# Kernel tuning notes

Hardware: AMD Instinct MI355X
Metric: run time of the kernel (lower is better)

The kernel has to match this reference:

```python
import jax, jax.numpy as jnp
import numpy as np

GROUPS = 32
EPS = 1e-5


def setup_inputs() -> dict:
    key = jax.random.key(0)
    ks = jax.random.split(key, 11)
    B, C, H, W = 64, 256, 32, 32
    s = 1.0 / np.sqrt(C)  # conv1d k=1 init scale
    inp = {
        'x': jax.random.normal(ks[0], (B, C, H, W), jnp.float32),
        'gn_weight': jnp.ones((C,), jnp.float32),
        'gn_bias': jnp.zeros((C,), jnp.float32),
        'wq': jax.random.uniform(ks[1], (C, C), jnp.float32, -s, s),
        'bq': jax.random.uniform(ks[2], (C,), jnp.float32, -s, s),
        'wk': jax.random.uniform(ks[3], (C, C), jnp.float32, -s, s),
        'bk': jax.random.uniform(ks[4], (C,), jnp.float32, -s, s),
        'wv': jax.random.uniform(ks[5], (C, C), jnp.float32, -s, s),
        'bv': jax.random.uniform(ks[6], (C,), jnp.float32, -s, s),
        'wo': jax.random.uniform(ks[7], (C, C), jnp.float32, -s, s),
        'bo': jax.random.uniform(ks[8], (C,), jnp.float32, -s, s),
    }
    return inp


def _group_norm(x, weight, bias):
    # x: (B, C, H, W); normalize per (group-channels, H, W)
    B, C, H, W = x.shape
    xg = x.reshape(B, GROUPS, C // GROUPS, H, W)
    mean = xg.mean(axis=(2, 3, 4), keepdims=True)
    var = xg.var(axis=(2, 3, 4), keepdims=True)
    xg = (xg - mean) * jax.lax.rsqrt(var + EPS)
    xn = xg.reshape(B, C, H, W)
    return xn * weight[None, :, None, None] + bias[None, :, None, None]


def reference(x, gn_weight, gn_bias, wq, bq, wk, bk, wv, bv, wo, bo):
    B, C, H, W = x.shape
    h = _group_norm(x, gn_weight, gn_bias).reshape(B, C, H * W)  # (B,C,N)
    # 1x1 conv1d == per-position linear over channels
    q = jnp.einsum('oc,bcn->bon', wq, h) + bq[None, :, None]
    k = jnp.einsum('oc,bcn->bon', wk, h) + bk[None, :, None]
    v = jnp.einsum('oc,bcn->bon', wv, h) + bv[None, :, None]
    scores = jnp.einsum('bcn,bcm->bnm', q, k) * (C ** -0.5)  # (B,N,N)
    weights = jax.nn.softmax(scores, axis=-1)
    attn = jnp.einsum('bnm,bcm->bcn', weights, v)  # (B,C,N)
    out = jnp.einsum('oc,bcn->bon', wo, attn) + bo[None, :, None]
    return x + out.reshape(B, C, H, W)
```

## Files before the change

kernel.cpp:

```cpp
#include <hip/hip_runtime.h>


#define BB 64
#define CC 256
#define NN 1024

typedef float  floatx4  __attribute__((ext_vector_type(4)));
typedef short  shortx8  __attribute__((ext_vector_type(8)));
typedef unsigned short ushortx4 __attribute__((ext_vector_type(4)));
typedef unsigned short ushortx8 __attribute__((ext_vector_type(8)));

__device__ __forceinline__ unsigned short f2bf(float f) {
  union { float f; unsigned int u; } cv; cv.f = f;
  unsigned int u = cv.u;
  u += 0x7fffu + ((u >> 16) & 1u);
  return (unsigned short)(u >> 16);
}

__device__ __forceinline__ floatx4 mfma16(shortx8 a, shortx8 b, floatx4 c) {
  return __builtin_amdgcn_mfma_f32_16x16x32_bf16(a, b, c, 0, 0, 0);
}

__device__ __forceinline__ void gload16(const unsigned short* g, unsigned short* s) {
  __builtin_amdgcn_global_load_lds(
      reinterpret_cast<const __attribute__((address_space(1))) void*>(
          (unsigned long long)g),
      reinterpret_cast<__attribute__((address_space(3))) void*>(
          (unsigned int)(unsigned long long)s),
      16, 0, 0);
}

__device__ __forceinline__ void barrier_raw() {
  asm volatile("" ::: "memory");
  __builtin_amdgcn_s_barrier();
  asm volatile("" ::: "memory");
}

__device__ __forceinline__ void bar_lds() {
  asm volatile("s_waitcnt lgkmcnt(0)" ::: "memory");
  __builtin_amdgcn_sched_barrier(0);
  barrier_raw();
}

__device__ __forceinline__ int sigma32(int r) {
  return (((r >> 2) & 3) << 3) + (((r >> 4) & 1) << 2) + (r & 3);
}

__global__ __launch_bounds__(256) void gn_kernel(const float* __restrict__ x,
                                                 const float* __restrict__ gw,
                                                 const float* __restrict__ gb,
                                                 unsigned short* __restrict__ h_t,
                                                 const float* __restrict__ wq, const float* __restrict__ bq,
                                                 const float* __restrict__ wk, const float* __restrict__ bk,
                                                 const float* __restrict__ wv, const float* __restrict__ bv,
                                                 const float* __restrict__ wo,
                                                 unsigned short* __restrict__ wqkv,
                                                 unsigned short* __restrict__ wo_bf,
                                                 float* __restrict__ bqkv) {
  if (blockIdx.x >= 32) {
    int cid = (blockIdx.x - 32) * 64 + blockIdx.y;
    int i = cid * 256 + threadIdx.x;
    if (i < 196608) {
      int o = i >> 8, c = i & 255;
      float val;
      if (o < 256)      val = wq[o * 256 + c] * 0.0625f;
      else if (o < 512) val = wk[(o - 256) * 256 + c];
      else              val = wv[(o - 512) * 256 + c];
      wqkv[i] = f2bf(val);
    } else if (i < 262144) {
      int j = i - 196608;
      wo_bf[j] = f2bf(wo[j]);
    } else if (i < 262912) {
      int o = i - 262144;
      float val;
      if (o < 256)      val = bq[o] * 0.0625f;
      else if (o < 512) val = bk[o - 256];
      else              val = bv[o - 512];
      bqkv[o] = val;
    }
    return;
  }
  int g = blockIdx.x, b = blockIdx.y;
  int t = threadIdx.x;
  const float* xb = x + ((size_t)b * CC + g * 8) * NN;

  float vals[8][4];
  float s = 0.f, sq = 0.f;
#pragma unroll
  for (int cc = 0; cc < 8; cc++) {
    floatx4 v4 = *(const floatx4*)(xb + cc * NN + t * 4);
#pragma unroll
    for (int j = 0; j < 4; j++) {
      vals[cc][j] = v4[j];
      s += v4[j];
      sq += v4[j] * v4[j];
    }
  }
#pragma unroll
  for (int d = 1; d < 64; d <<= 1) {
    s  += __shfl_xor(s, d);
    sq += __shfl_xor(sq, d);
  }
  __shared__ float ssum[4], ssq[4];
  int w = t >> 6;
  if ((t & 63) == 0) { ssum[w] = s; ssq[w] = sq; }
  __syncthreads();
  s  = ssum[0] + ssum[1] + ssum[2] + ssum[3];
  sq = ssq[0] + ssq[1] + ssq[2] + ssq[3];
  float mean = s * (1.f / 8192.f);
  float var  = sq * (1.f / 8192.f) - mean * mean;
  float rstd = rsqrtf(var + 1e-5f);

  float gam[8], bet[8];
#pragma unroll
  for (int cc = 0; cc < 8; cc++) {
    float gm = gw[g * 8 + cc] * rstd;
    gam[cc] = gm;
    bet[cc] = gb[g * 8 + cc] - mean * gm;
  }
  unsigned short* hb = h_t + (size_t)b * NN * CC + g * 8;
#pragma unroll
  for (int j = 0; j < 4; j++) {
    ushortx8 pk;
#pragma unroll
    for (int cc = 0; cc < 8; cc++) pk[cc] = f2bf(vals[cc][j] * gam[cc] + bet[cc]);
    *(ushortx8*)(hb + (size_t)(t * 4 + j) * CC) = pk;
  }
}

__global__ __launch_bounds__(512, 4) void qkv_gemm(const unsigned short* __restrict__ h_t,
                                                   const unsigned short* __restrict__ wqkv,
                                                   const float* __restrict__ bqkv,
                                                   unsigned short* __restrict__ q_t,
                                                   unsigned short* __restrict__ k_t,
                                                   unsigned short* __restrict__ v) {
  __shared__ __align__(16) unsigned short sM[32768];
  __shared__ __align__(16) unsigned short sRep[32 * 136];
  int rb = blockIdx.x, b = blockIdx.y;
  int t = threadIdx.x, w = t >> 6, l = t & 63, lo = l & 15, h = l >> 4;
  int rowg = w >> 1, colg = w & 1;
  const unsigned short* A = h_t + ((size_t)b * NN + rb * 128) * CC;

  int srow_w = w * 2 + (l >> 5);
  int schunk = l & 31;

#pragma unroll
  for (int i = 0; i < 8; i++) {
    int row = i * 16 + srow_w;
    gload16(A + (size_t)row * CC + ((schunk ^ (row & 7)) << 3),
            &sM[(i * 16 + w * 2) << 8]);
  }
  asm volatile("s_waitcnt vmcnt(0)" ::: "memory");
  barrier_raw();

  shortx8 a[2][8];
#pragma unroll
  for (int i = 0; i < 2; i++) {
    int row = rowg * 32 + i * 16 + lo;
#pragma unroll
    for (int ch = 0; ch < 8; ch++)
      a[i][ch] = *(const shortx8*)(&sM[(row << 8) + (((ch * 4 + h) ^ (row & 7)) << 3)]);
  }
  bar_lds();

#pragma unroll
  for (int i = 0; i < 4; i++) {
    int row = i * 16 + srow_w;
    gload16(wqkv + (size_t)row * CC + ((schunk ^ (row & 7)) << 3),
            &sM[(i * 16 + w * 2) << 8]);
  }

  floatx4 zero4 = {0.f, 0.f, 0.f, 0.f};
  for (int c = 0; c < 12; c++) {
    int cb = (c & 1) << 14;
    if (c < 11) {
      int nb = ((c + 1) & 1) << 14;
#pragma unroll
      for (int i = 0; i < 4; i++) {
        int row = i * 16 + srow_w;
        gload16(wqkv + (size_t)((c + 1) * 64 + row) * CC + ((schunk ^ (row & 7)) << 3),
                &sM[nb + ((i * 16 + w * 2) << 8)]);
      }
      asm volatile("s_waitcnt vmcnt(4)" ::: "memory");
    } else {
      asm volatile("s_waitcnt vmcnt(0)" ::: "memory");
    }
    barrier_raw();

    floatx4 acc[2][2];
    acc[0][0] = zero4; acc[0][1] = zero4; acc[1][0] = zero4; acc[1][1] = zero4;
    int r0 = colg * 32 + lo, r1 = colg * 32 + 16 + lo;
    __builtin_amdgcn_s_setprio(1);
#pragma unroll
    for (int ch = 0; ch < 8; ch++) {
      shortx8 b0 = *(const shortx8*)(&sM[cb + (r0 << 8) + (((ch * 4 + h) ^ (r0 & 7)) << 3)]);
      shortx8 b1 = *(const shortx8*)(&sM[cb + (r1 << 8) + (((ch * 4 + h) ^ (r1 & 7)) << 3)]);
      acc[0][0] = mfma16(a[0][ch], b0, acc[0][0]);
      acc[0][1] = mfma16(a[0][ch], b1, acc[0][1]);
      acc[1][0] = mfma16(a[1][ch], b0, acc[1][0]);
      acc[1][1] = mfma16(a[1][ch], b1, acc[1][1]);
    }
    __builtin_amdgcn_s_setprio(0);

    if (c < 8) {
      unsigned short* dst = (c < 4) ? q_t : k_t;
      bar_lds();
      unsigned short* sQK = &sM[cb];
#pragma unroll
      for (int i = 0; i < 2; i++) {
#pragma unroll
        for (int j = 0; j < 2; j++) {
          float bias = bqkv[(c << 6) + colg * 32 + j * 16 + lo];
          int o_l = colg * 32 + j * 16 + lo;
#pragma unroll
          for (int r = 0; r < 4; r++) {
            int n_l = rowg * 32 + i * 16 + h * 4 + r;
            sQK[n_l * 72 + o_l] = f2bf(acc[i][j][r] + bias);
          }
        }
      }
      bar_lds();
#pragma unroll
      for (int p = 0; p < 2; p++) {
        int slot = p * 512 + t;
        int n_l = slot >> 3, sg = (slot & 7) << 3;
        ushortx8 vv = *(const ushortx8*)(&sQK[n_l * 72 + sg]);
        *(ushortx8*)(dst + ((size_t)b * NN + rb * 128 + n_l) * CC + ((c & 3) << 6) + sg) = vv;
      }
      bar_lds();
    } else {
      int vch0 = (c - 8) << 6;
#pragma unroll
      for (int half = 0; half < 2; half++) {
        if (colg == half) {
#pragma unroll
          for (int i = 0; i < 2; i++) {
#pragma unroll
            for (int j = 0; j < 2; j++) {
              float bias = bqkv[512 + vch0 + half * 32 + j * 16 + lo];
              ushortx4 pk;
#pragma unroll
              for (int r = 0; r < 4; r++) pk[r] = f2bf(acc[i][j][r] + bias);
              *(ushortx4*)(&sRep[(j * 16 + lo) * 136 + rowg * 32 + i * 16 + h * 4]) = pk;
            }
          }
        }
        bar_lds();
        int o_l = t >> 4, nseg = (t & 15) << 3;
        ushortx8 vv = *(const ushortx8*)(&sRep[o_l * 136 + nseg]);
        *(ushortx8*)(v + ((size_t)b * CC + vch0 + half * 32 + o_l) * NN + rb * 128 + nseg) = vv;
        bar_lds();
      }
    }
  }
}

__global__ __launch_bounds__(512, 2) void flash_kernel(const unsigned short* __restrict__ q_t,
                                                       const unsigned short* __restrict__ k_t,
                                                       const unsigned short* __restrict__ v,
                                                       unsigned short* __restrict__ attn_t) {
  __shared__ __align__(16) unsigned short sMem[32768];
  int bid = blockIdx.x;
  int wgid = ((bid & 7) << 5) + (bid >> 3);
  int b = wgid >> 2, qblk = wgid & 3;
  int t = threadIdx.x, w = t >> 6, l = t & 63, lo = l & 15, h = l >> 4;
  const unsigned short* qtb = q_t + (size_t)b * NN * CC;
  const unsigned short* ktb = k_t + (size_t)b * NN * CC;
  const unsigned short* vb  = v   + (size_t)b * CC * NN;
  int qbase = qblk * 256 + w * 32;

  shortx8 qfA[8], qfB[8];
#pragma unroll
  for (int ch = 0; ch < 8; ch++) {
    qfA[ch] = *(const shortx8*)(qtb + (size_t)(qbase + lo) * CC + ch * 32 + h * 8);
    qfB[ch] = *(const shortx8*)(qtb + (size_t)(qbase + 16 + lo) * CC + ch * 32 + h * 8);
  }

  floatx4 zero4 = {0.f, 0.f, 0.f, 0.f};
  floatx4 oA[16], oB[16];
#pragma unroll
  for (int i = 0; i < 16; i++) { oA[i] = zero4; oB[i] = zero4; }
  float mA = -1e30f, lsA = 0.f, mB = -1e30f, lsB = 0.f;

  int krow_l = (w << 2) + (l >> 5);
  int kchunk = l & 31;
  int vrow_l = (w << 5) + (l >> 2);
  int vchunk = l & 3;

#pragma unroll
  for (int i = 0; i < 2; i++) {
    int row = krow_l + i * 2;
    gload16(ktb + (size_t)sigma32(row) * CC + ((kchunk ^ (row & 7)) << 3),
            &sMem[((w << 2) + i * 2) << 8]);
  }
#pragma unroll
  for (int i = 0; i < 2; i++) {
    int row = vrow_l + i * 16;
    gload16(vb + (size_t)row * NN + ((vchunk ^ ((row >> 1) & 3)) << 3),
            &sMem[16384 + (((w << 5) + i * 16) << 5)]);
  }

  for (int kb = 0; kb < 32; kb++) {
    int cur = kb & 1;
    int kB = cur << 13;
    int vB = 16384 + (cur << 13);
    if (kb < 31) {
      int nxt = cur ^ 1, k0n = (kb + 1) << 5;
#pragma unroll
      for (int i = 0; i < 2; i++) {
        int row = krow_l + i * 2;
        gload16(ktb + (size_t)(k0n + sigma32(row)) * CC + ((kchunk ^ (row & 7)) << 3),
                &sMem[(nxt << 13) + (((w << 2) + i * 2) << 8)]);
      }
#pragma unroll
      for (int i = 0; i < 2; i++) {
        int row = vrow_l + i * 16;
        gload16(vb + (size_t)row * NN + k0n + ((vchunk ^ ((row >> 1) & 3)) << 3),
                &sMem[16384 + (nxt << 13) + (((w << 5) + i * 16) << 5)]);
      }
      asm volatile("s_waitcnt vmcnt(4)" ::: "memory");
    } else {
      asm volatile("s_waitcnt vmcnt(0)" ::: "memory");
    }
    barrier_raw();

    floatx4 sA[2], sB[2];
#pragma unroll
    for (int i = 0; i < 2; i++) { sA[i] = zero4; sB[i] = zero4; }
    __builtin_amdgcn_s_setprio(1);
#pragma unroll
    for (int kt = 0; kt < 2; kt++) {
      const unsigned short* kp = &sMem[kB + ((kt * 16 + lo) << 8)];
#pragma unroll
      for (int ch = 0; ch < 8; ch++) {
        shortx8 kf = *(const shortx8*)(kp + (((ch * 4 + h) ^ (lo & 7)) << 3));
        sA[kt] = mfma16(kf, qfA[ch], sA[kt]);
        sB[kt] = mfma16(kf, qfB[ch], sB[kt]);
      }
    }
    __builtin_amdgcn_s_setprio(0);

    unsigned int pkA[2][2], pkB[2][2];
    {
      float pmax = fmaxf(fmaxf(fmaxf(sA[0][0], sA[0][1]), fmaxf(sA[0][2], sA[0][3])),
                         fmaxf(fmaxf(sA[1][0], sA[1][1]), fmaxf(sA[1][2], sA[1][3])));
      if (!__all(pmax - mA <= 8.f)) {
        pmax = fmaxf(pmax, __shfl_xor(pmax, 16));
        pmax = fmaxf(pmax, __shfl_xor(pmax, 32));
        float mn = fmaxf(mA, pmax);
        float alpha = __expf(mA - mn);
        mA = mn;
        lsA *= alpha;
#pragma unroll
        for (int r = 0; r < 4; r++) {
          float ar = __shfl(alpha, (h << 4) + (h << 2) + r);
#pragma unroll
          for (int cbi = 0; cbi < 16; cbi++) oA[cbi][r] *= ar;
        }
      }
      float rs = 0.f;
#pragma unroll
      for (int kt = 0; kt < 2; kt++) {
        float p0 = __expf(sA[kt][0] - mA);
        float p1 = __expf(sA[kt][1] - mA);
        float p2 = __expf(sA[kt][2] - mA);
        float p3 = __expf(sA[kt][3] - mA);
        rs += (p0 + p1) + (p2 + p3);
        pkA[kt][0] = (unsigned)f2bf(p0) | ((unsigned)f2bf(p1) << 16);
        pkA[kt][1] = (unsigned)f2bf(p2) | ((unsigned)f2bf(p3) << 16);
      }
      lsA += rs;
    }
    {
      float pmax = fmaxf(fmaxf(fmaxf(sB[0][0], sB[0][1]), fmaxf(sB[0][2], sB[0][3])),
                         fmaxf(fmaxf(sB[1][0], sB[1][1]), fmaxf(sB[1][2], sB[1][3])));
      if (!__all(pmax - mB <= 8.f)) {
        pmax = fmaxf(pmax, __shfl_xor(pmax, 16));
        pmax = fmaxf(pmax, __shfl_xor(pmax, 32));
        float mn = fmaxf(mB, pmax);
        float alpha = __expf(mB - mn);
        mB = mn;
        lsB *= alpha;
#pragma unroll
        for (int r = 0; r < 4; r++) {
          float ar = __shfl(alpha, (h << 4) + (h << 2) + r);
#pragma unroll
          for (int cbi = 0; cbi < 16; cbi++) oB[cbi][r] *= ar;
        }
      }
      float rs = 0.f;
#pragma unroll
      for (int kt = 0; kt < 2; kt++) {
        float p0 = __expf(sB[kt][0] - mB);
        float p1 = __expf(sB[kt][1] - mB);
        float p2 = __expf(sB[kt][2] - mB);
        float p3 = __expf(sB[kt][3] - mB);
        rs += (p0 + p1) + (p2 + p3);
        pkB[kt][0] = (unsigned)f2bf(p0) | ((unsigned)f2bf(p1) << 16);
        pkB[kt][1] = (unsigned)f2bf(p2) | ((unsigned)f2bf(p3) << 16);
      }
      lsB += rs;
    }

    {
      union { unsigned int u[4]; shortx8 v; } paA, paB;
      paA.u[0] = pkA[0][0]; paA.u[1] = pkA[0][1];
      paA.u[2] = pkA[1][0]; paA.u[3] = pkA[1][1];
      paB.u[0] = pkB[0][0]; paB.u[1] = pkB[0][1];
      paB.u[2] = pkB[1][0]; paB.u[3] = pkB[1][1];
      __builtin_amdgcn_s_setprio(1);
#pragma unroll
      for (int cbi = 0; cbi < 16; cbi++) {
        int row = (cbi << 4) + lo;
        shortx8 vf = *(const shortx8*)(&sMem[vB + (row << 5) +
                                             ((h ^ ((row >> 1) & 3)) << 3)]);
        oA[cbi] = mfma16(paA.v, vf, oA[cbi]);
        oB[cbi] = mfma16(paB.v, vf, oB[cbi]);
      }
      __builtin_amdgcn_s_setprio(0);
    }
    barrier_raw();
  }

  lsA += __shfl_xor(lsA, 16);
  lsA += __shfl_xor(lsA, 32);
  lsB += __shfl_xor(lsB, 16);
  lsB += __shfl_xor(lsB, 32);

  float rlA[4], rlB[4];
#pragma unroll
  for (int r = 0; r < 4; r++) {
    rlA[r] = 1.f / __shfl(lsA, (h << 4) + (h << 2) + r);
    rlB[r] = 1.f / __shfl(lsB, (h << 4) + (h << 2) + r);
  }
  unsigned short* ab = attn_t + (size_t)b * NN * CC;
  unsigned short* ow = &sMem[w << 12];

#pragma unroll
  for (int cbi = 0; cbi < 16; cbi++) {
#pragma unroll
    for (int r = 0; r < 4; r++) {
      int q = (h << 2) + r;
      int c = (cbi << 4) + lo;
      int sw = (q ^ (q >> 3)) & 7;
      ow[(q << 8) + (((c >> 3) ^ sw) << 3) + (lo & 7)] = f2bf(oA[cbi][r] * rlA[r]);
    }
  }
  bar_lds();
#pragma unroll
  for (int it = 0; it < 8; it++) {
    int q = (it << 1) + (l >> 5);
    int gc = l & 31;
    int sw = (q ^ (q >> 3)) & 7;
    ushortx8 vv = *(const ushortx8*)(&ow[(q << 8) + ((gc ^ sw) << 3)]);
    *(ushortx8*)(ab + (size_t)(qbase + q) * CC + (gc << 3)) = vv;
  }
  bar_lds();
#pragma unroll
  for (int cbi = 0; cbi < 16; cbi++) {
#pragma unroll
    for (int r = 0; r < 4; r++) {
      int q = (h << 2) + r;
      int c = (cbi << 4) + lo;
      int sw = (q ^ (q >> 3)) & 7;
      ow[(q << 8) + (((c >> 3) ^ sw) << 3) + (lo & 7)] = f2bf(oB[cbi][r] * rlB[r]);
    }
  }
  bar_lds();
#pragma unroll
  for (int it = 0; it < 8; it++) {
    int q = (it << 1) + (l >> 5);
    int gc = l & 31;
    int sw = (q ^ (q >> 3)) & 7;
    ushortx8 vv = *(const ushortx8*)(&ow[(q << 8) + ((gc ^ sw) << 3)]);
    *(ushortx8*)(ab + (size_t)(qbase + 16 + q) * CC + (gc << 3)) = vv;
  }
}

__global__ __launch_bounds__(512, 4) void outproj_gemm(const unsigned short* __restrict__ attn_t,
                                                       const unsigned short* __restrict__ wo_bf,
                                                       const float* __restrict__ bo,
                                                       const float* __restrict__ x,
                                                       float* __restrict__ out) {
  __shared__ __align__(16) unsigned short sM[32768];
  __shared__ __align__(16) float sRepF[16 * 132];
  int rb = blockIdx.x, b = blockIdx.y;
  int t = threadIdx.x, w = t >> 6, l = t & 63, lo = l & 15, h = l >> 4;
  int rowg = w >> 1, colg = w & 1;
  const unsigned short* A = attn_t + ((size_t)b * NN + rb * 128) * CC;

  int srow_w = w * 2 + (l >> 5);
  int schunk = l & 31;

#pragma unroll
  for (int i = 0; i < 8; i++) {
    int row = i * 16 + srow_w;
    gload16(A + (size_t)row * CC + ((schunk ^ (row & 7)) << 3),
            &sM[(i * 16 + w * 2) << 8]);
  }
  asm volatile("s_waitcnt vmcnt(0)" ::: "memory");
  barrier_raw();

  shortx8 a[2][8];
#pragma unroll
  for (int i = 0; i < 2; i++) {
    int row = rowg * 32 + i * 16 + lo;
#pragma unroll
    for (int ch = 0; ch < 8; ch++)
      a[i][ch] = *(const shortx8*)(&sM[(row << 8) + (((ch * 4 + h) ^ (row & 7)) << 3)]);
  }
  bar_lds();

#pragma unroll
  for (int i = 0; i < 4; i++) {
    int row = i * 16 + srow_w;
    gload16(wo_bf + (size_t)row * CC + ((schunk ^ (row & 7)) << 3),
            &sM[(i * 16 + w * 2) << 8]);
  }

  floatx4 zero4 = {0.f, 0.f, 0.f, 0.f};
  for (int c = 0; c < 4; c++) {
    int cb = (c & 1) << 14;
    if (c < 3) {
      int nb = ((c + 1) & 1) << 14;
#pragma unroll
      for (int i = 0; i < 4; i++) {
        int row = i * 16 + srow_w;
        gload16(wo_bf + (size_t)((c + 1) * 64 + row) * CC + ((schunk ^ (row & 7)) << 3),
                &sM[nb + ((i * 16 + w * 2) << 8)]);
      }
      asm volatile("s_waitcnt vmcnt(4)" ::: "memory");
    } else {
      asm volatile("s_waitcnt vmcnt(0)" ::: "memory");
    }
    barrier_raw();

    floatx4 acc[2][2];
    acc[0][0] = zero4; acc[0][1] = zero4; acc[1][0] = zero4; acc[1][1] = zero4;
    int r0 = colg * 32 + lo, r1 = colg * 32 + 16 + lo;
    __builtin_amdgcn_s_setprio(1);
#pragma unroll
    for (int ch = 0; ch < 8; ch++) {
      shortx8 b0 = *(const shortx8*)(&sM[cb + (r0 << 8) + (((ch * 4 + h) ^ (r0 & 7)) << 3)]);
      shortx8 b1 = *(const shortx8*)(&sM[cb + (r1 << 8) + (((ch * 4 + h) ^ (r1 & 7)) << 3)]);
      acc[0][0] = mfma16(a[0][ch], b0, acc[0][0]);
      acc[0][1] = mfma16(a[0][ch], b1, acc[0][1]);
      acc[1][0] = mfma16(a[1][ch], b0, acc[1][0]);
      acc[1][1] = mfma16(a[1][ch], b1, acc[1][1]);
    }
    __builtin_amdgcn_s_setprio(0);

#pragma unroll
    for (int quarter = 0; quarter < 4; quarter++) {
      int j = quarter & 1;
      if (colg == (quarter >> 1)) {
        float bias = bo[(c << 6) + quarter * 16 + lo];
#pragma unroll
        for (int i = 0; i < 2; i++) {
          floatx4 val;
#pragma unroll
          for (int r = 0; r < 4; r++) val[r] = acc[i][j][r] + bias;
          *(floatx4*)(&sRepF[lo * 132 + rowg * 32 + i * 16 + h * 4]) = val;
        }
      }
      bar_lds();
      int o_l = t >> 5, nq = (t & 31) << 2;
      floatx4 rep = *(const floatx4*)(&sRepF[o_l * 132 + nq]);
      size_t idx = ((size_t)b * CC + (c << 6) + quarter * 16 + o_l) * NN + rb * 128 + nq;
      floatx4 xr = *(const floatx4*)(x + idx);
#pragma unroll
      for (int r = 0; r < 4; r++) rep[r] += xr[r];
      *(floatx4*)(out + idx) = rep;
      bar_lds();
    }
  }
}

extern "C" void kernel_launch(void* const* d_in, const int* in_sizes, int n_in,
                              void* d_out, int out_size, void* d_ws, size_t ws_size,
                              hipStream_t stream) {
  const float* x  = (const float*)d_in[0];
  const float* gw = (const float*)d_in[1];
  const float* gb = (const float*)d_in[2];
  const float* wq = (const float*)d_in[3];
  const float* bq = (const float*)d_in[4];
  const float* wk = (const float*)d_in[5];
  const float* bk = (const float*)d_in[6];
  const float* wv = (const float*)d_in[7];
  const float* bv = (const float*)d_in[8];
  const float* wo = (const float*)d_in[9];
  const float* bo = (const float*)d_in[10];
  float* out = (float*)d_out;

  char* ws = (char*)d_ws;
  unsigned short* q_t   = (unsigned short*)(ws);
  unsigned short* k_t   = (unsigned short*)(ws + 33554432);
  unsigned short* v     = (unsigned short*)(ws + 67108864);
  unsigned short* h_t   = (unsigned short*)(ws + 100663296);
  unsigned short* wqkv  = (unsigned short*)(ws + 134217728);
  unsigned short* wo_bf = (unsigned short*)(ws + 134610944);
  float*          bqkv  = (float*)(ws + 134742016);
  unsigned short* attn_t = h_t;

  gn_kernel<<<dim3(49, 64), dim3(256), 0, stream>>>(x, gw, gb, h_t,
                                                    wq, bq, wk, bk, wv, bv, wo,
                                                    wqkv, wo_bf, bqkv);
  qkv_gemm<<<dim3(8, 64), dim3(512), 0, stream>>>(h_t, wqkv, bqkv, q_t, k_t, v);
  flash_kernel<<<dim3(256), dim3(512), 0, stream>>>(q_t, k_t, v, attn_t);
  outproj_gemm<<<dim3(8, 64), dim3(512), 0, stream>>>(attn_t, wo_bf, bo, x, out);
}
```

Baseline: 189.0 us.

## Quad-buffer K/V tiles and process two key tiles per barrier in flash kernel

The flash attention loop changes from a double-buffered 32-key step to four LDS buffers, handling two 32-key tiles per iteration. This prefetches two tiles ahead and halves the number of barriers and wait points per key sweep. The cost is doubling shared memory to 128 KB per block, which cannot fit two blocks per CU as the launch bounds request, so occupancy likely drops to one block per CU. It also adds register pressure from the extra score accumulators.

```diff
diff --git a/kernel.cpp b/kernel.cpp
--- a/kernel.cpp
+++ b/kernel.cpp
@@ -259,7 +259,7 @@
                                                        const unsigned short* __restrict__ k_t,
                                                        const unsigned short* __restrict__ v,
                                                        unsigned short* __restrict__ attn_t) {
-  __shared__ __align__(16) unsigned short sMem[32768];
+  __shared__ __align__(16) unsigned short sMem[65536];
   int bid = blockIdx.x;
   int wgid = ((bid & 7) << 5) + (bid >> 3);
   int b = wgid >> 2, qblk = wgid & 3;
@@ -288,62 +288,83 @@
   int vchunk = l & 3;
 
 #pragma unroll
-  for (int i = 0; i < 2; i++) {
-    int row = krow_l + i * 2;
-    gload16(ktb + (size_t)sigma32(row) * CC + ((kchunk ^ (row & 7)) << 3),
-            &sMem[((w << 2) + i * 2) << 8]);
-  }
-#pragma unroll
-  for (int i = 0; i < 2; i++) {
-    int row = vrow_l + i * 16;
-    gload16(vb + (size_t)row * NN + ((vchunk ^ ((row >> 1) & 3)) << 3),
-            &sMem[16384 + (((w << 5) + i * 16) << 5)]);
-  }
-
-  for (int kb = 0; kb < 32; kb++) {
-    int cur = kb & 1;
-    int kB = cur << 13;
-    int vB = 16384 + (cur << 13);
-    if (kb < 31) {
-      int nxt = cur ^ 1, k0n = (kb + 1) << 5;
-#pragma unroll
-      for (int i = 0; i < 2; i++) {
-        int row = krow_l + i * 2;
-        gload16(ktb + (size_t)(k0n + sigma32(row)) * CC + ((kchunk ^ (row & 7)) << 3),
-                &sMem[(nxt << 13) + (((w << 2) + i * 2) << 8)]);
-      }
-#pragma unroll
-      for (int i = 0; i < 2; i++) {
-        int row = vrow_l + i * 16;
-        gload16(vb + (size_t)row * NN + k0n + ((vchunk ^ ((row >> 1) & 3)) << 3),
-                &sMem[16384 + (nxt << 13) + (((w << 5) + i * 16) << 5)]);
-      }
-      asm volatile("s_waitcnt vmcnt(4)" ::: "memory");
+  for (int tt = 0; tt < 2; tt++) {
+    int k0 = tt << 5;
+#pragma unroll
+    for (int i = 0; i < 2; i++) {
+      int row = krow_l + i * 2;
+      gload16(ktb + (size_t)(k0 + sigma32(row)) * CC + ((kchunk ^ (row & 7)) << 3),
+              &sMem[(tt << 13) + (((w << 2) + i * 2) << 8)]);
+    }
+#pragma unroll
+    for (int i = 0; i < 2; i++) {
+      int row = vrow_l + i * 16;
+      gload16(vb + (size_t)row * NN + k0 + ((vchunk ^ ((row >> 1) & 3)) << 3),
+              &sMem[32768 + (tt << 13) + (((w << 5) + i * 16) << 5)]);
+    }
+  }
+
+  for (int j = 0; j < 16; j++) {
+    if (j < 15) {
+#pragma unroll
+      for (int tt = 0; tt < 2; tt++) {
+        int kbn = 2 * j + 2 + tt;
+        int k0n = kbn << 5;
+        int bufn = kbn & 3;
+#pragma unroll
+        for (int i = 0; i < 2; i++) {
+          int row = krow_l + i * 2;
+          gload16(ktb + (size_t)(k0n + sigma32(row)) * CC + ((kchunk ^ (row & 7)) << 3),
+                  &sMem[(bufn << 13) + (((w << 2) + i * 2) << 8)]);
+        }
+#pragma unroll
+        for (int i = 0; i < 2; i++) {
+          int row = vrow_l + i * 16;
+          gload16(vb + (size_t)row * NN + k0n + ((vchunk ^ ((row >> 1) & 3)) << 3),
+                  &sMem[32768 + (bufn << 13) + (((w << 5) + i * 16) << 5)]);
+        }
+      }
+      asm volatile("s_waitcnt vmcnt(8)" ::: "memory");
     } else {
       asm volatile("s_waitcnt vmcnt(0)" ::: "memory");
     }
     barrier_raw();
 
-    floatx4 sA[2], sB[2];
-#pragma unroll
-    for (int i = 0; i < 2; i++) { sA[i] = zero4; sB[i] = zero4; }
+    int kBa = ((2 * j) & 3) << 13;
+    int kBb = ((2 * j + 1) & 3) << 13;
+    int vBa = 32768 + (((2 * j) & 3) << 13);
+    int vBb = 32768 + (((2 * j + 1) & 3) << 13);
+
+    floatx4 sAa[2], sBa[2], sAb[2], sBb[2];
+#pragma unroll
+    for (int i = 0; i < 2; i++) { sAa[i] = zero4; sBa[i] = zero4; sAb[i] = zero4; sBb[i] = zero4; }
     __builtin_amdgcn_s_setprio(1);
 #pragma unroll
     for (int kt = 0; kt < 2; kt++) {
-      const unsigned short* kp = &sMem[kB + ((kt * 16 + lo) << 8)];
+      const unsigned short* kp = &sMem[kBa + ((kt * 16 + lo) << 8)];
 #pragma unroll
       for (int ch = 0; ch < 8; ch++) {
         shortx8 kf = *(const shortx8*)(kp + (((ch * 4 + h) ^ (lo & 7)) << 3));
-        sA[kt] = mfma16(kf, qfA[ch], sA[kt]);
-        sB[kt] = mfma16(kf, qfB[ch], sB[kt]);
+        sAa[kt] = mfma16(kf, qfA[ch], sAa[kt]);
+        sBa[kt] = mfma16(kf, qfB[ch], sBa[kt]);
+      }
+    }
+#pragma unroll
+    for (int kt = 0; kt < 2; kt++) {
+      const unsigned short* kp = &sMem[kBb + ((kt * 16 + lo) << 8)];
+#pragma unroll
+      for (int ch = 0; ch < 8; ch++) {
+        shortx8 kf = *(const shortx8*)(kp + (((ch * 4 + h) ^ (lo & 7)) << 3));
+        sAb[kt] = mfma16(kf, qfA[ch], sAb[kt]);
+        sBb[kt] = mfma16(kf, qfB[ch], sBb[kt]);
       }
     }
     __builtin_amdgcn_s_setprio(0);
 
-    unsigned int pkA[2][2], pkB[2][2];
+    unsigned int pkAa[2][2], pkBa[2][2], pkAb[2][2], pkBb[2][2];
     {
-      float pmax = fmaxf(fmaxf(fmaxf(sA[0][0], sA[0][1]), fmaxf(sA[0][2], sA[0][3])),
-                         fmaxf(fmaxf(sA[1][0], sA[1][1]), fmaxf(sA[1][2], sA[1][3])));
+      float pmax = fmaxf(fmaxf(fmaxf(sAa[0][0], sAa[0][1]), fmaxf(sAa[0][2], sAa[0][3])),
+                         fmaxf(fmaxf(sAa[1][0], sAa[1][1]), fmaxf(sAa[1][2], sAa[1][3])));
       if (!__all(pmax - mA <= 8.f)) {
         pmax = fmaxf(pmax, __shfl_xor(pmax, 16));
         pmax = fmaxf(pmax, __shfl_xor(pmax, 32));
@@ -361,19 +382,19 @@
       float rs = 0.f;
 #pragma unroll
       for (int kt = 0; kt < 2; kt++) {
-        float p0 = __expf(sA[kt][0] - mA);
-        float p1 = __expf(sA[kt][1] - mA);
-        float p2 = __expf(sA[kt][2] - mA);
-        float p3 = __expf(sA[kt][3] - mA);
+        float p0 = __expf(sAa[kt][0] - mA);
+        float p1 = __expf(sAa[kt][1] - mA);
+        float p2 = __expf(sAa[kt][2] - mA);
+        float p3 = __expf(sAa[kt][3] - mA);
         rs += (p0 + p1) + (p2 + p3);
-        pkA[kt][0] = (unsigned)f2bf(p0) | ((unsigned)f2bf(p1) << 16);
-        pkA[kt][1] = (unsigned)f2bf(p2) | ((unsigned)f2bf(p3) << 16);
+        pkAa[kt][0] = (unsigned)f2bf(p0) | ((unsigned)f2bf(p1) << 16);
+        pkAa[kt][1] = (unsigned)f2bf(p2) | ((unsigned)f2bf(p3) << 16);
       }
       lsA += rs;
     }
     {
-      float pmax = fmaxf(fmaxf(fmaxf(sB[0][0], sB[0][1]), fmaxf(sB[0][2], sB[0][3])),
-                         fmaxf(fmaxf(sB[1][0], sB[1][1]), fmaxf(sB[1][2], sB[1][3])));
+      float pmax = fmaxf(fmaxf(fmaxf(sBa[0][0], sBa[0][1]), fmaxf(sBa[0][2], sBa[0][3])),
+                         fmaxf(fmaxf(sBa[1][0], sBa[1][1]), fmaxf(sBa[1][2], sBa[1][3])));
       if (!__all(pmax - mB <= 8.f)) {
         pmax = fmaxf(pmax, __shfl_xor(pmax, 16));
         pmax = fmaxf(pmax, __shfl_xor(pmax, 32));
@@ -391,28 +412,104 @@
       float rs = 0.f;
 #pragma unroll
       for (int kt = 0; kt < 2; kt++) {
-        float p0 = __expf(sB[kt][0] - mB);
-        float p1 = __expf(sB[kt][1] - mB);
-        float p2 = __expf(sB[kt][2] - mB);
-        float p3 = __expf(sB[kt][3] - mB);
+        float p0 = __expf(sBa[kt][0] - mB);
+        float p1 = __expf(sBa[kt][1] - mB);
+        float p2 = __expf(sBa[kt][2] - mB);
+        float p3 = __expf(sBa[kt][3] - mB);
         rs += (p0 + p1) + (p2 + p3);
-        pkB[kt][0] = (unsigned)f2bf(p0) | ((unsigned)f2bf(p1) << 16);
-        pkB[kt][1] = (unsigned)f2bf(p2) | ((unsigned)f2bf(p3) << 16);
+        pkBa[kt][0] = (unsigned)f2bf(p0) | ((unsigned)f2bf(p1) << 16);
+        pkBa[kt][1] = (unsigned)f2bf(p2) | ((unsigned)f2bf(p3) << 16);
       }
       lsB += rs;
     }
-
     {
       union { unsigned int u[4]; shortx8 v; } paA, paB;
-      paA.u[0] = pkA[0][0]; paA.u[1] = pkA[0][1];
-      paA.u[2] = pkA[1][0]; paA.u[3] = pkA[1][1];
-      paB.u[0] = pkB[0][0]; paB.u[1] = pkB[0][1];
-      paB.u[2] = pkB[1][0]; paB.u[3] = pkB[1][1];
+      paA.u[0] = pkAa[0][0]; paA.u[1] = pkAa[0][1];
+      paA.u[2] = pkAa[1][0]; paA.u[3] = pkAa[1][1];
+      paB.u[0] = pkBa[0][0]; paB.u[1] = pkBa[0][1];
+      paB.u[2] = pkBa[1][0]; paB.u[3] = pkBa[1][1];
       __builtin_amdgcn_s_setprio(1);
 #pragma unroll
       for (int cbi = 0; cbi < 16; cbi++) {
         int row = (cbi << 4) + lo;
-        shortx8 vf = *(const shortx8*)(&sMem[vB + (row << 5) +
+        shortx8 vf = *(const shortx8*)(&sMem[vBa + (row << 5) +
+                                             ((h ^ ((row >> 1) & 3)) << 3)]);
+        oA[cbi] = mfma16(paA.v, vf, oA[cbi]);
+        oB[cbi] = mfma16(paB.v, vf, oB[cbi]);
+      }
+      __builtin_amdgcn_s_setprio(0);
+    }
+    {
+      float pmax = fmaxf(fmaxf(fmaxf(sAb[0][0], sAb[0][1]), fmaxf(sAb[0][2], sAb[0][3])),
+                         fmaxf(fmaxf(sAb[1][0], sAb[1][1]), fmaxf(sAb[1][2], sAb[1][3])));
+      if (!__all(pmax - mA <= 8.f)) {
+        pmax = fmaxf(pmax, __shfl_xor(pmax, 16));
+        pmax = fmaxf(pmax, __shfl_xor(pmax, 32));
+        float mn = fmaxf(mA, pmax);
+        float alpha = __expf(mA - mn);
+        mA = mn;
+        lsA *= alpha;
+#pragma unroll
+        for (int r = 0; r < 4; r++) {
+          float ar = __shfl(alpha, (h << 4) + (h << 2) + r);
+#pragma unroll
+          for (int cbi = 0; cbi < 16; cbi++) oA[cbi][r] *= ar;
+        }
+      }
+      float rs = 0.f;
+#pragma unroll
+      for (int kt = 0; kt < 2; kt++) {
+        float p0 = __expf(sAb[kt][0] - mA);
+        float p1 = __expf(sAb[kt][1] - mA);
+        float p2 = __expf(sAb[kt][2] - mA);
+        float p3 = __expf(sAb[kt][3] - mA);
+        rs += (p0 + p1) + (p2 + p3);
+        pkAb[kt][0] = (unsigned)f2bf(p0) | ((unsigned)f2bf(p1) << 16);
+        pkAb[kt][1] = (unsigned)f2bf(p2) | ((unsigned)f2bf(p3) << 16);
+      }
+      lsA += rs;
+    }
+    {
+      float pmax = fmaxf(fmaxf(fmaxf(sBb[0][0], sBb[0][1]), fmaxf(sBb[0][2], sBb[0][3])),
+                         fmaxf(fmaxf(sBb[1][0], sBb[1][1]), fmaxf(sBb[1][2], sBb[1][3])));
+      if (!__all(pmax - mB <= 8.f)) {
+        pmax = fmaxf(pmax, __shfl_xor(pmax, 16));
+        pmax = fmaxf(pmax, __shfl_xor(pmax, 32));
+        float mn = fmaxf(mB, pmax);
+        float alpha = __expf(mB - mn);
+        mB = mn;
+        lsB *= alpha;
+#pragma unroll
+        for (int r = 0; r < 4; r++) {
+          float ar = __shfl(alpha, (h << 4) + (h << 2) + r);
+#pragma unroll
+          for (int cbi = 0; cbi < 16; cbi++) oB[cbi][r] *= ar;
+        }
+      }
+      float rs = 0.f;
+#pragma unroll
+      for (int kt = 0; kt < 2; kt++) {
+        float p0 = __expf(sBb[kt][0] - mB);
+        float p1 = __expf(sBb[kt][1] - mB);
+        float p2 = __expf(sBb[kt][2] - mB);
+        float p3 = __expf(sBb[kt][3] - mB);
+        rs += (p0 + p1) + (p2 + p3);
+        pkBb[kt][0] = (unsigned)f2bf(p0) | ((unsigned)f2bf(p1) << 16);
+        pkBb[kt][1] = (unsigned)f2bf(p2) | ((unsigned)f2bf(p3) << 16);
+      }
+      lsB += rs;
+    }
+    {
+      union { unsigned int u[4]; shortx8 v; } paA, paB;
+      paA.u[0] = pkAb[0][0]; paA.u[1] = pkAb[0][1];
+      paA.u[2] = pkAb[1][0]; paA.u[3] = pkAb[1][1];
+      paB.u[0] = pkBb[0][0]; paB.u[1] = pkBb[0][1];
+      paB.u[2] = pkBb[1][0]; paB.u[3] = pkBb[1][1];
+      __builtin_amdgcn_s_setprio(1);
+#pragma unroll
+      for (int cbi = 0; cbi < 16; cbi++) {
+        int row = (cbi << 4) + lo;
+        shortx8 vf = *(const shortx8*)(&sMem[vBb + (row << 5) +
                                              ((h ^ ((row >> 1) & 3)) << 3)]);
         oA[cbi] = mfma16(paA.v, vf, oA[cbi]);
         oB[cbi] = mfma16(paB.v, vf, oB[cbi]);
```

After: 219.5 us. 16.1% more time.
